# Optimization experiments

Measured on AMD Instinct MI355X. Metric: run time of the kernel, lower is better.

## Reference

```python
import jax, jax.numpy as jnp
import numpy as np

NTIME, NBATCH = 1024, 65536


def setup_inputs() -> dict:
    key = jax.random.key(0)
    k1, k2, k3 = jax.random.split(key, 3)
    # times must be sorted along the time axis (dim 0) per batch column
    times = jnp.sort(jax.random.uniform(k1, (NTIME, NBATCH), dtype=jnp.float32), axis=0)
    values = jax.random.normal(k2, (NTIME, NBATCH), dtype=jnp.float32)
    # query times inside the covered range (0,1)
    t = jax.random.uniform(k3, (NBATCH,), dtype=jnp.float32)
    return {"times": times, "values": values, "t": t}


def reference(times, values, t):
    # times, values: (ntime, nbatch); t: (nbatch,)
    ntime, nbatch = times.shape
    # precached slopes as in __init__: (ntime-1, nbatch)
    slopes = jnp.diff(values, axis=0) / jnp.diff(times, axis=0)
    # searchsorted-by-counting: number of knots <= t, wrapped mod ntime
    gi = jnp.mod(jnp.sum((times - t[None, :]) <= 0, axis=0), ntime)  # (nbatch,)
    b = jnp.arange(nbatch)
    # torch negative-index wrap semantics: gi-1 == -1 wraps to last row
    iv = jnp.mod(gi - 1, ntime)       # index into times/values
    isl = jnp.mod(gi - 1, ntime - 1)  # index into slopes
    # direct per-batch gather (equivalent to torch.diagonal(x[gi-1]))
    v0 = values[iv, b]
    s0 = slopes[isl, b]
    t0 = times[iv, b]
    return v0 + s0 * (t - t0)
```

## Files before the change

kernel.cpp:

```cpp
#include <hip/hip_runtime.h>

__global__ void bts_interp_kernel(const float* __restrict__ times,
                                  const float* __restrict__ values,
                                  const float* __restrict__ t,
                                  float* __restrict__ out,
                                  int ntime, int nbatch) {
    int b = blockIdx.x * blockDim.x + threadIdx.x;
    if (b >= nbatch) return;

    float tq = t[b];

    int lo = 0, hi = ntime;
    float t0v = 0.0f;
    float t1v = 0.0f;
    while (lo < hi) {
        int mid = (lo + hi) >> 1;
        float v = times[(long)mid * nbatch + b];
        if (v <= tq) { lo = mid + 1; t0v = v; }
        else         { hi = mid;     t1v = v; }
    }

    float res;
    if (lo > 0 && lo < ntime) {
        long base = (long)(lo - 1) * nbatch + b;
        float va = values[base];
        float vb = values[base + nbatch];
        res = va + (vb - va) / (t1v - t0v) * (tq - t0v);
    } else {
        long base = (long)(ntime - 2) * nbatch + b;
        float ta = times[base];
        float tb = times[base + nbatch];
        float va = values[base];
        float vb = values[base + nbatch];
        res = vb + (vb - va) / (tb - ta) * (tq - tb);
    }
    out[b] = res;
}

extern "C" void kernel_launch(void* const* d_in, const int* in_sizes, int n_in,
                              void* d_out, int out_size, void* d_ws, size_t ws_size,
                              hipStream_t stream) {
    const float* times  = (const float*)d_in[0];
    const float* values = (const float*)d_in[1];
    const float* t      = (const float*)d_in[2];
    float* out = (float*)d_out;

    int nbatch = in_sizes[2];
    int ntime  = in_sizes[0] / nbatch;

    const int BLOCK = 256;
    int grid = (nbatch + BLOCK - 1) / BLOCK;
    bts_interp_kernel<<<grid, BLOCK, 0, stream>>>(times, values, t, out, ntime, nbatch);
}
```

Before: 407.1 us.

## Replace dependent binary search with guessed window and parallel multi-probe stages

The serial binary search over the time axis is replaced by a staged search. First it guesses a 256-row window from tq*ntime and probes 8 points in it at once. A short binary search runs only while the bracket is wider than 32, then 7 probes at stride 4 and 4 consecutive probes, each group issued in parallel. This swaps a long chain of dependent global loads for a few rounds of independent loads, at the cost of more total loads per thread. The initial guess assumes roughly uniform knot times, but the bracket logic stays correct for any sorted input.

```diff
diff --git a/kernel.cpp b/kernel.cpp
--- a/kernel.cpp
+++ b/kernel.cpp
@@ -1,37 +1,91 @@
 #include <hip/hip_runtime.h>
 
-__global__ void bts_interp_kernel(const float* __restrict__ times,
-                                  const float* __restrict__ values,
-                                  const float* __restrict__ t,
-                                  float* __restrict__ out,
-                                  int ntime, int nbatch) {
+__global__ void __launch_bounds__(256) bts_interp_kernel(
+        const float* __restrict__ times,
+        const float* __restrict__ values,
+        const float* __restrict__ t,
+        float* __restrict__ out,
+        int ntime, int nbatch) {
     int b = blockIdx.x * blockDim.x + threadIdx.x;
     if (b >= nbatch) return;
 
+    const long stride = (long)nbatch;
     float tq = t[b];
 
     int lo = 0, hi = ntime;
     float t0v = 0.0f;
     float t1v = 0.0f;
-    while (lo < hi) {
+
+    if (ntime >= 256) {
+        int g = (int)(tq * (float)ntime);
+        int W = g - 112;
+        if (W < 0) W = 0;
+        if (W > ntime - 256) W = ntime - 256;
+        float pv[8];
+#pragma unroll
+        for (int i = 0; i < 8; ++i)
+            pv[i] = times[(long)(W + 32 * i) * stride + b];
+#pragma unroll
+        for (int i = 0; i < 8; ++i) {
+            int p = W + 32 * i;
+            if (pv[i] <= tq) { int nl = p + 1; if (nl > lo) { lo = nl; t0v = pv[i]; } }
+            else if (p < hi) { hi = p; t1v = pv[i]; }
+        }
+    }
+
+    while (hi - lo > 32) {
         int mid = (lo + hi) >> 1;
-        float v = times[(long)mid * nbatch + b];
+        float v = times[(long)mid * stride + b];
         if (v <= tq) { lo = mid + 1; t0v = v; }
         else         { hi = mid;     t1v = v; }
     }
 
+    {
+        int base = lo;
+        int pi[7]; float pv[7];
+#pragma unroll
+        for (int i = 0; i < 7; ++i) {
+            int p = base + 4 * (i + 1);
+            if (p > ntime - 1) p = ntime - 1;
+            pi[i] = p;
+            pv[i] = times[(long)p * stride + b];
+        }
+#pragma unroll
+        for (int i = 0; i < 7; ++i) {
+            if (pv[i] <= tq) { int nl = pi[i] + 1; if (nl > lo) { lo = nl; t0v = pv[i]; } }
+            else if (pi[i] < hi) { hi = pi[i]; t1v = pv[i]; }
+        }
+    }
+
+    {
+        int base = lo;
+        int pi[4]; float pv[4];
+#pragma unroll
+        for (int i = 0; i < 4; ++i) {
+            int p = base + i;
+            if (p > ntime - 1) p = ntime - 1;
+            pi[i] = p;
+            pv[i] = times[(long)p * stride + b];
+        }
+#pragma unroll
+        for (int i = 0; i < 4; ++i) {
+            if (pv[i] <= tq) { int nl = pi[i] + 1; if (nl > lo) { lo = nl; t0v = pv[i]; } }
+            else if (pi[i] < hi) { hi = pi[i]; t1v = pv[i]; }
+        }
+    }
+
     float res;
     if (lo > 0 && lo < ntime) {
-        long base = (long)(lo - 1) * nbatch + b;
-        float va = values[base];
-        float vb = values[base + nbatch];
+        long base2 = (long)(lo - 1) * stride + b;
+        float va = values[base2];
+        float vb = values[base2 + stride];
         res = va + (vb - va) / (t1v - t0v) * (tq - t0v);
     } else {
-        long base = (long)(ntime - 2) * nbatch + b;
-        float ta = times[base];
-        float tb = times[base + nbatch];
-        float va = values[base];
-        float vb = values[base + nbatch];
+        long base2 = (long)(ntime - 2) * stride + b;
+        float ta = times[base2];
+        float tb = times[base2 + stride];
+        float va = values[base2];
+        float vb = values[base2 + stride];
         res = vb + (vb - va) / (tb - ta) * (tq - tb);
     }
     out[b] = res;
```

Result: slower. 425.0 us (+4.4%).

## Use one wavefront per column with two-level ballot search and XCD block swizzle

Applied to the files above, without the earlier changes.

Replaces the per-thread 10-step dependent binary search with a wavefront-cooperative search. Each of the 64 lanes samples a strided knot, a ballot and popcount picks the segment, and a second ballot over that segment finds the exact interval, with neighbouring knots taken by shuffle. The goal is to cut the long chain of dependent global loads down to two levels. Block indices are also remapped so adjacent columns run on the same XCD and share L2 lines. The cost is many more cache-line requests per column, since 4 columns per block means lanes touch many rows. A fallback kernel is kept for shapes that do not fit.

```diff
diff --git a/kernel.cpp b/kernel.cpp
--- a/kernel.cpp
+++ b/kernel.cpp
@@ -1,25 +1,72 @@
 #include <hip/hip_runtime.h>
 
-__global__ void bts_interp_kernel(const float* __restrict__ times,
-                                  const float* __restrict__ values,
-                                  const float* __restrict__ t,
-                                  float* __restrict__ out,
-                                  int ntime, int nbatch) {
+__global__ void __launch_bounds__(256) bts_interp_wave(
+        const float* __restrict__ times,
+        const float* __restrict__ values,
+        const float* __restrict__ t,
+        float* __restrict__ out,
+        int ntime, int nbatch, int s1, int cpx) {
+    int lane = threadIdx.x & 63;
+    int bid  = blockIdx.x;
+    if (cpx > 0) bid = (bid & 7) * cpx + (bid >> 3);
+    int col = bid * 4 + (threadIdx.x >> 6);
+    if (col >= nbatch) return;
+
+    const long stride = nbatch;
+    float tq = t[col];
+
+    float v1 = times[(long)(lane * s1) * stride + col];
+    unsigned long long m1 = __ballot(v1 <= tq);
+    int c = __popcll(m1);
+
+    int lo;
+    float t0 = 0.0f, t1 = 0.0f;
+    if (c == 0) {
+        lo = 0;
+    } else {
+        int base = (c - 1) * s1;
+        float v2 = 0.0f;
+        if (lane < s1) v2 = times[(long)(base + lane) * stride + col];
+        unsigned long long m2 = __ballot((lane < s1) && (v2 <= tq));
+        int d = __popcll(m2);
+        lo = base + d;
+        t0 = __shfl(v2, d - 1);
+        if (d < s1)      t1 = __shfl(v2, d);
+        else if (c < 64) t1 = __shfl(v1, c);
+    }
+
+    float res;
+    if (lo > 0 && lo < ntime) {
+        long p = (long)(lo - 1) * stride + col;
+        float va = values[p];
+        float vb = values[p + stride];
+        res = va + (vb - va) / (t1 - t0) * (tq - t0);
+    } else {
+        long p = (long)(ntime - 2) * stride + col;
+        float ta = times[p], tb = times[p + stride];
+        float va = values[p], vb = values[p + stride];
+        res = vb + (vb - va) / (tb - ta) * (tq - tb);
+    }
+    if (lane == 0) out[col] = res;
+}
+
+__global__ void bts_interp_fallback(const float* __restrict__ times,
+                                    const float* __restrict__ values,
+                                    const float* __restrict__ t,
+                                    float* __restrict__ out,
+                                    int ntime, int nbatch) {
     int b = blockIdx.x * blockDim.x + threadIdx.x;
     if (b >= nbatch) return;
 
     float tq = t[b];
-
     int lo = 0, hi = ntime;
-    float t0v = 0.0f;
-    float t1v = 0.0f;
+    float t0v = 0.0f, t1v = 0.0f;
     while (lo < hi) {
         int mid = (lo + hi) >> 1;
         float v = times[(long)mid * nbatch + b];
         if (v <= tq) { lo = mid + 1; t0v = v; }
         else         { hi = mid;     t1v = v; }
     }
-
     float res;
     if (lo > 0 && lo < ntime) {
         long base = (long)(lo - 1) * nbatch + b;
@@ -48,7 +95,16 @@
     int nbatch = in_sizes[2];
     int ntime  = in_sizes[0] / nbatch;
 
-    const int BLOCK = 256;
-    int grid = (nbatch + BLOCK - 1) / BLOCK;
-    bts_interp_kernel<<<grid, BLOCK, 0, stream>>>(times, values, t, out, ntime, nbatch);
+    if (ntime >= 64 && ntime % 64 == 0 && (ntime / 64) <= 64) {
+        int s1 = ntime / 64;
+        int nblocks = (nbatch + 3) / 4;
+        int cpx = (nblocks % 8 == 0) ? (nblocks / 8) : 0;
+        bts_interp_wave<<<nblocks, 256, 0, stream>>>(times, values, t, out,
+                                                     ntime, nbatch, s1, cpx);
+    } else {
+        const int BLOCK = 256;
+        int grid = (nbatch + BLOCK - 1) / BLOCK;
+        bts_interp_fallback<<<grid, BLOCK, 0, stream>>>(times, values, t, out,
+                                                        ntime, nbatch);
+    }
 }
```

New measurement: 459.1 us. 1.13x slower.

## Replace full binary search with coarse strided scan plus short refinement

Applied to the files above, without the earlier changes.

The first search phase reads every 8th time row with independent, unrolled loads. A running count and bracket values locate the coarse interval. A binary search over at most 8 rows then finds the exact knot. This swaps about ten dependent, latency-bound global loads per thread for many independent coalesced loads, at the cost of reading far more data. A fallback kernel handles ntime values that are not a multiple of 8 or are too small.

```diff
diff --git a/kernel.cpp b/kernel.cpp
--- a/kernel.cpp
+++ b/kernel.cpp
@@ -1,25 +1,83 @@
 #include <hip/hip_runtime.h>
 
-__global__ void bts_interp_kernel(const float* __restrict__ times,
-                                  const float* __restrict__ values,
-                                  const float* __restrict__ t,
-                                  float* __restrict__ out,
-                                  int ntime, int nbatch) {
+#define SUB 8
+
+__global__ void __launch_bounds__(256) bts_scan_kernel(
+        const float* __restrict__ times,
+        const float* __restrict__ values,
+        const float* __restrict__ t,
+        float* __restrict__ out,
+        int ntime, int nbatch) {
+    int b = blockIdx.x * blockDim.x + threadIdx.x;
+    if (b >= nbatch) return;
+
+    const long stride = nbatch;
+    float tq = t[b];
+
+    int nsub = ntime / SUB;
+    int cs = 0;
+    float t0s = 0.0f;
+    float t1s = __builtin_inff();
+    const float* p = times + b;
+    const long rstep = (long)SUB * stride;
+#pragma unroll 16
+    for (int k = 0; k < nsub; ++k) {
+        float v = p[(long)k * rstep];
+        bool le = (v <= tq);
+        cs += le ? 1 : 0;
+        t0s = le ? v : t0s;
+        t1s = (!le && v < t1s) ? v : t1s;
+    }
+
+    int lo, hi;
+    float t0v = t0s, t1v = t1s;
+    if (cs == 0) {
+        lo = 0; hi = 0;
+    } else {
+        lo = SUB * (cs - 1) + 1;
+        hi = SUB * cs;
+    }
+    while (lo < hi) {
+        int mid = (lo + hi) >> 1;
+        float v = times[(long)mid * stride + b];
+        if (v <= tq) { lo = mid + 1; t0v = v; }
+        else         { hi = mid;     t1v = v; }
+    }
+
+    float res;
+    if (lo > 0 && lo < ntime) {
+        long base = (long)(lo - 1) * stride + b;
+        float va = values[base];
+        float vb = values[base + stride];
+        res = va + (vb - va) / (t1v - t0v) * (tq - t0v);
+    } else {
+        long base = (long)(ntime - 2) * stride + b;
+        float ta = times[base];
+        float tb = times[base + stride];
+        float va = values[base];
+        float vb = values[base + stride];
+        res = vb + (vb - va) / (tb - ta) * (tq - tb);
+    }
+    out[b] = res;
+}
+
+__global__ void bts_interp_fallback(const float* __restrict__ times,
+                                    const float* __restrict__ values,
+                                    const float* __restrict__ t,
+                                    float* __restrict__ out,
+                                    int ntime, int nbatch) {
     int b = blockIdx.x * blockDim.x + threadIdx.x;
     if (b >= nbatch) return;
 
     float tq = t[b];
-
     int lo = 0, hi = ntime;
-    float t0v = 0.0f;
-    float t1v = 0.0f;
+    float t0v = 0.0f, t1v = 0.0f;
     while (lo < hi) {
         int mid = (lo + hi) >> 1;
         float v = times[(long)mid * nbatch + b];
         if (v <= tq) { lo = mid + 1; t0v = v; }
         else         { hi = mid;     t1v = v; }
     }
-
     float res;
     if (lo > 0 && lo < ntime) {
         long base = (long)(lo - 1) * nbatch + b;
@@ -50,5 +108,11 @@
 
     const int BLOCK = 256;
     int grid = (nbatch + BLOCK - 1) / BLOCK;
-    bts_interp_kernel<<<grid, BLOCK, 0, stream>>>(times, values, t, out, ntime, nbatch);
+    if (ntime >= 2 * SUB && ntime % SUB == 0) {
+        bts_scan_kernel<<<grid, BLOCK, 0, stream>>>(times, values, t, out,
+                                                    ntime, nbatch);
+    } else {
+        bts_interp_fallback<<<grid, BLOCK, 0, stream>>>(times, values, t, out,
+                                                        ntime, nbatch);
+    }
 }
```

New measurement: 407.7 us. About the same (+0.1%).
